# Optimization experiments

Hardware: AMD Instinct MI355X
Metric: run time of the kernel (lower is better)

The kernel has to match this reference:

```python
import jax, jax.numpy as jnp
import numpy as np

B, N, D = 4, 256, 256
H, DH = 4, 64
INNER = H * DH
L, MULT, EDGE, KNN = 2, 2, 11, 3
LN_EPS = 1e-5


def _layernorm(x, w, b):
    m = x.mean(-1, keepdims=True)
    v = ((x - m) ** 2).mean(-1, keepdims=True)
    return (x - m) * jax.lax.rsqrt(v + LN_EPS) * w + b


def _gelu(x):
    return jax.nn.gelu(x, approximate=False)  # torch nn.GELU default = exact erf


def _knn_pair_mask(coords, valid, k):
    # coords [B,M,2], valid [B,M] -> symmetric KNN adjacency among neighbors
    Bm, M = valid.shape
    d = jnp.sqrt(jnp.sum((coords[:, :, None, :] - coords[:, None, :, :]) ** 2, -1))
    eye = jnp.eye(M, dtype=bool)[None]
    inv = ~(valid[:, :, None] & valid[:, None, :])
    d = jnp.where(inv | eye, jnp.inf, d)
    neg, idx = jax.lax.top_k(-d, k)  # k smallest distances
    finite = jnp.isfinite(neg)
    bi = jnp.arange(Bm)[:, None, None]
    ri = jnp.arange(M)[None, :, None]
    mask = jnp.zeros((Bm, M, M), bool).at[bi, ri, idx].set(finite)
    mask = mask | jnp.swapaxes(mask, 1, 2)
    return mask & ~eye


def _build_graph(x, coords):
    # valid node mask (infer_valid_node_mask) and hop ids (infer_hop_ids)
    valid = (jnp.abs(x).sum(-1) > 0).at[:, 0].set(True)
    hop = jnp.ones((B, N), jnp.int32).at[:, 0].set(0)
    hop = hop.at[:, 1 + (N - 1) // 2:].set(2)
    eye = jnp.eye(N, dtype=bool)[None]
    adj = jnp.broadcast_to(eye, (B, N, N))
    nv = valid[:, 1:]
    adj = adj.at[:, 0, 1:].set(nv)
    adj = adj.at[:, 1:, 0].set(nv)
    npm = _knn_pair_mask(coords[:, 1:], nv, min(KNN, N - 2))
    adj = adj.at[:, 1:, 1:].set(adj[:, 1:, 1:] | npm)
    vp = valid[:, :, None] & valid[:, None, :]
    adj = adj & (vp | eye)
    # edge features [B,N,N,11]
    rel = coords[:, None, :, :] - coords[:, :, None, :]  # coords[j]-coords[i]
    dx, dy = rel[..., 0], rel[..., 1]
    dist = jnp.sqrt(dx ** 2 + dy ** 2 + 1e-8)
    cdist = jnp.sqrt(coords[..., 0] ** 2 + coords[..., 1] ** 2 + 1e-8)
    nvm = valid.at[:, 0].set(False)
    cd = jnp.where(nvm, cdist, 0.0)
    cnt = jnp.clip(nvm.sum(-1), 1).astype(x.dtype)
    ls = cd.sum(-1) / cnt
    ls = jnp.where(ls > 0, ls, 1.0)
    ndist = dist / jnp.clip(ls, 1e-6)[:, None, None]
    idx = jnp.arange(N)
    ones2 = jnp.ones((N, N), bool)
    qic = (idx[:, None] == 0) & ones2
    kic = (idx[None, :] == 0) & ones2
    eye2 = jnp.eye(N, dtype=bool)
    isnn = ~(qic | kic | eye2)
    same_hop = hop[:, :, None] == hop[:, None, :]
    hop_delta = jnp.abs(hop[:, None, :] - hop[:, :, None]).astype(x.dtype)
    same_ct = jnp.zeros((B, N, N), x.dtype)  # cell_inf is None
    f = lambda m: jnp.broadcast_to(m.astype(x.dtype), (B, N, N))
    edge_attr = jnp.stack(
        [dx, dy, dist, ndist, f(qic), f(kic), f(eye2), f(isnn),
         same_hop.astype(x.dtype), hop_delta, same_ct], -1)
    return adj, edge_attr


def _forward(x, coords, Wq, Wk, Wv, eb_w1, eb_b1, eb_w2, eb_b2,
             ev_w1, ev_b1, ev_w2, ev_b2, Wo, bo,
             ln1_w, ln1_b, ln2_w, ln2_b, ff_w1, ff_b1, ff_w2, ff_b2):
    adj, e = _build_graph(x, coords)
    scale = DH ** -0.5
    big = jnp.finfo(x.dtype).max
    for l in range(L):
        xn = _layernorm(x, ln1_w[l], ln1_b[l])
        q = (xn @ Wq[l]).reshape(B, N, H, DH).transpose(0, 2, 1, 3)  # b h n d
        k = (xn @ Wk[l]).reshape(B, N, H, DH).transpose(0, 2, 1, 3)
        v = (xn @ Wv[l]).reshape(B, N, H, DH).transpose(0, 2, 1, 3)
        eb = _gelu(e @ eb_w1[l] + eb_b1[l]) @ eb_w2[l] + eb_b2[l]  # [B,N,N,H]
        ev = _gelu(e @ ev_w1[l] + ev_b1[l]) @ ev_w2[l] + ev_b2[l]  # [B,N,N,INNER]
        ev = ev.reshape(B, N, N, H, DH).transpose(0, 3, 1, 2, 4)   # b h i j d
        sim = jnp.einsum('bhid,bhjd->bhij', q, k) * scale + eb.transpose(0, 3, 1, 2)
        sim = jnp.where(adj[:, None], sim, -big)
        attn = jax.nn.softmax(sim, -1)
        msgs = v[:, :, None, :, :] + ev                            # value injection
        out = jnp.einsum('bhij,bhijd->bhid', attn, msgs)
        out = out.transpose(0, 2, 1, 3).reshape(B, N, INNER) @ Wo[l] + bo[l]
        x = x + out
        xn2 = _layernorm(x, ln2_w[l], ln2_b[l])
        hg = xn2 @ ff_w1[l] + ff_b1[l]
        a, g = jnp.split(hg, 2, -1)  # GEGLU
        x = x + ((a * _gelu(g)) @ ff_w2[l] + ff_b2[l])
    return x


def setup_inputs() -> dict:
    key = jax.random.key(0)
    ks = iter(jax.random.split(key, 32))
    w = lambda shape, s=0.05: jax.random.normal(next(ks), shape, jnp.float32) * s
    return {
        'x': jax.random.normal(next(ks), (B, N, D), jnp.float32),
        'coords': jax.random.normal(next(ks), (B, N, 2), jnp.float32) * 3.0,
        'Wq': w((L, D, INNER)), 'Wk': w((L, D, INNER)), 'Wv': w((L, D, INNER)),
        'eb_w1': w((L, EDGE, INNER)), 'eb_b1': jnp.zeros((L, INNER)),
        'eb_w2': w((L, INNER, H)), 'eb_b2': jnp.zeros((L, H)),
        'ev_w1': w((L, EDGE, INNER)), 'ev_b1': jnp.zeros((L, INNER)),
        'ev_w2': w((L, INNER, INNER)), 'ev_b2': jnp.zeros((L, INNER)),
        'Wo': w((L, INNER, D)), 'bo': jnp.zeros((L, D)),
        'ln1_w': jnp.ones((L, D)), 'ln1_b': jnp.zeros((L, D)),
        'ln2_w': jnp.ones((L, D)), 'ln2_b': jnp.zeros((L, D)),
        'ff_w1': w((L, D, 2 * MULT * D)), 'ff_b1': jnp.zeros((L, 2 * MULT * D)),
        'ff_w2': w((L, MULT * D, D)), 'ff_b2': jnp.zeros((L, D)),
    }


def reference(x, coords, Wq, Wk, Wv, eb_w1, eb_b1, eb_w2, eb_b2,
              ev_w1, ev_b1, ev_w2, ev_b2, Wo, bo,
              ln1_w, ln1_b, ln2_w, ln2_b, ff_w1, ff_b1, ff_w2, ff_b2):
    return _forward(x, coords, Wq, Wk, Wv, eb_w1, eb_b1, eb_w2, eb_b2,
                    ev_w1, ev_b1, ev_w2, ev_b2, Wo, bo,
                    ln1_w, ln1_b, ln2_w, ln2_b, ff_w1, ff_b1, ff_w2, ff_b2)
```

## Files before the change

kernel.cpp:

```cpp
#include <hip/hip_runtime.h>


#define MAXE  16384
#define NONX  22080
#define BF16_TOTAL 1441792

typedef __attribute__((ext_vector_type(8))) short bf16x8;
typedef __attribute__((ext_vector_type(4))) float f32x4;

struct PtrPack { const void* p[23]; };

__device__ __forceinline__ float bf2f(unsigned short s) {
  return __uint_as_float(((unsigned)s) << 16);
}
__device__ __forceinline__ unsigned short f2bf(float f) {
  unsigned u = __float_as_uint(f);
  u += 0x7fffu + ((u >> 16) & 1u);
  return (unsigned short)(u >> 16);
}
__device__ __forceinline__ float gelu_f(float x) {
  return 0.5f * x * (1.0f + erff(x * 0.70710678118654752440f));
}
__device__ __forceinline__ float wave_red_sum(float v) {
#pragma unroll
  for (int o = 32; o > 0; o >>= 1) v += __shfl_xor(v, o);
  return v;
}

__device__ __forceinline__ void edge_feats(int i, int j, float cxi, float cyi,
                                           float cxj, float cyj, float lsd, float* e) {
  float dx = cxj - cxi, dy = cyj - cyi;
  float dist = sqrtf(dx * dx + dy * dy + 1e-8f);
  e[0] = dx; e[1] = dy; e[2] = dist; e[3] = dist / lsd;
  bool qic = (i == 0), kic = (j == 0), eye = (i == j);
  e[4] = qic ? 1.f : 0.f;
  e[5] = kic ? 1.f : 0.f;
  e[6] = eye ? 1.f : 0.f;
  e[7] = (!qic && !kic && !eye) ? 1.f : 0.f;
  int hi = (i == 0) ? 0 : ((i < 128) ? 1 : 2);
  int hj = (j == 0) ? 0 : ((j < 128) ? 1 : 2);
  e[8] = (hi == hj) ? 1.f : 0.f;
  int hd = hj - hi;
  e[9] = (float)(hd < 0 ? -hd : hd);
}

__global__ __launch_bounds__(256) void k_convert(PtrPack pp, float* __restrict__ blobF,
                                                 unsigned short* __restrict__ blobB,
                                                 int* __restrict__ valid,
                                                 float* __restrict__ rowsum,
                                                 int* __restrict__ gctr) {
  bool isf32 = (*(const unsigned*)pp.p[15] == 0x3F800000u);
  int t = threadIdx.x;
  if (blockIdx.x == 0 && t == 0) *gctr = 0;
  if (blockIdx.x < 1024) {
    if (blockIdx.x < 32) rowsum[blockIdx.x * 256 + t] = 0.f;
    int r = blockIdx.x;
    int idx = r * 256 + t;
    float v = isf32 ? ((const float*)pp.p[0])[idx]
                    : bf2f(((const unsigned short*)pp.p[0])[idx]);
    blobF[idx] = v;
    __shared__ float s[4];
    float a = wave_red_sum(fabsf(v));
    if ((t & 63) == 0) s[t >> 6] = a;
    __syncthreads();
    if (t == 0) valid[r] = ((s[0] + s[1] + s[2] + s[3]) > 0.0f) || ((r & 255) == 0);
  } else {
    const int fst[16] = {0,2048,7680,8192,10240,10304,15936,16448,16960,17472,17984,18496,19008,19520,21568,22080};
    const int fsz[15] = {2048,5632,512,2048,8,5632,512,512,512,512,512,512,512,2048,512};
    const int fin[15] = {1,5,6,7,8,9,10,12,14,15,16,17,18,20,22};
    const int bst[8]  = {0,131072,262144,393216,524288,655360,1179648,1441792};
    const int bin[7]  = {2,3,4,13,11,19,21};
    const int NUNITS = NONX + BF16_TOTAL / 4;
    for (int u = (blockIdx.x - 1024) * 256 + t; u < NUNITS; u += 1024 * 256) {
      if (u < NONX) {
        int s = 0;
        while (s < 14 && u >= fst[s + 1]) ++s;
        int e = u - fst[s];
        float v = 0.f;
        if (e < fsz[s]) v = isf32 ? ((const float*)pp.p[fin[s]])[e]
                                  : bf2f(((const unsigned short*)pp.p[fin[s]])[e]);
        blobF[262144 + u] = v;
      } else {
        int bi = (u - NONX) * 4;
        int s = 0;
        while (s < 6 && bi >= bst[s + 1]) ++s;
        int e = bi - bst[s];
        ushort4 o;
        if (isf32) {
          const float* sp = (const float*)pp.p[bin[s]] + e;
          o.x = f2bf(sp[0]); o.y = f2bf(sp[1]); o.z = f2bf(sp[2]); o.w = f2bf(sp[3]);
        } else {
          o = *(const ushort4*)((const unsigned short*)pp.p[bin[s]] + e);
        }
        *(ushort4*)&blobB[bi] = o;
      }
    }
  }
}

__global__ __launch_bounds__(256) void k_knn(const float* __restrict__ cf,
                                             const int* __restrict__ valid,
                                             int* __restrict__ knn) {
  int blk = blockIdx.x;
  int b = blk >> 6;
  int w = threadIdx.x >> 6, lane = threadIdx.x & 63;
  int i = (blk & 63) * 4 + w;
  const float2* cc = (const float2*)(cf + b * 512);
  float2 ci = cc[i];
  bool vi = (valid[b * 256 + i] != 0) && (i != 0);
  unsigned long long key[4];
#pragma unroll
  for (int k = 0; k < 4; ++k) {
    int j = lane + 64 * k;
    bool ok = vi && (j != 0) && (j != i) && (valid[b * 256 + j] != 0);
    unsigned long long kk = ~0ull;
    if (ok) {
      float2 cj = cc[j];
      float dx = ci.x - cj.x, dy = ci.y - cj.y;
      float dd = sqrtf(dx * dx + dy * dy);
      kk = (((unsigned long long)__float_as_uint(dd)) << 32) | (unsigned)j;
    }
    key[k] = kk;
  }
  int out[3];
#pragma unroll
  for (int rnd = 0; rnd < 3; ++rnd) {
    unsigned long long m = key[0];
    if (key[1] < m) m = key[1];
    if (key[2] < m) m = key[2];
    if (key[3] < m) m = key[3];
#pragma unroll
    for (int o = 32; o > 0; o >>= 1) {
      unsigned long long om = __shfl_xor(m, o);
      if (om < m) m = om;
    }
    out[rnd] = (m != ~0ull) ? (int)(m & 0xFFFFFFFFull) : -1;
#pragma unroll
    for (int k = 0; k < 4; ++k)
      if (key[k] == m) key[k] = ~0ull;
  }
  if (lane == 0) {
    knn[(b * 256 + i) * 3 + 0] = out[0];
    knn[(b * 256 + i) * 3 + 1] = out[1];
    knn[(b * 256 + i) * 3 + 2] = out[2];
  }
}

__global__ __launch_bounds__(256) void k_csr(const float* __restrict__ cf,
                                             const int* __restrict__ valid,
                                             const int* __restrict__ knn,
                                             float* __restrict__ lsbuf,
                                             int* __restrict__ deg, int* __restrict__ rowptr,
                                             int* __restrict__ rowof, int* __restrict__ colsb,
                                             int* __restrict__ gctr) {
  int b = blockIdx.x, t = threadIdx.x;
  __shared__ unsigned adjw[256][8];
  __shared__ float sred[8];
  __shared__ int wsum[4];
  __shared__ int sbase;

  int r = b * 256 + t;
  float cx = cf[r * 2 + 0], cy = cf[r * 2 + 1];
  int lv = valid[r];
#pragma unroll
  for (int w = 0; w < 8; ++w) adjw[t][w] = 0u;
  __syncthreads();

  atomicOr(&adjw[t][t >> 5], 1u << (t & 31));
  if (t >= 1 && lv) {
    atomicOr(&adjw[0][t >> 5], 1u << (t & 31));
    atomicOr(&adjw[t][0], 1u);
  }
#pragma unroll
  for (int s = 0; s < 3; ++s) {
    int j = knn[r * 3 + s];
    if (j >= 0) {
      atomicOr(&adjw[t][j >> 5], 1u << (j & 31));
      atomicOr(&adjw[j][t >> 5], 1u << (t & 31));
    }
  }
  float cdist = sqrtf(cx * cx + cy * cy + 1e-8f);
  int nvm = (t >= 1) && lv;
  float rs = wave_red_sum(nvm ? cdist : 0.0f);
  float rc = wave_red_sum(nvm ? 1.0f : 0.0f);
  if ((t & 63) == 0) { sred[t >> 6] = rs; sred[4 + (t >> 6)] = rc; }
  __syncthreads();

  if (t == 0) {
    float totd = sred[0] + sred[1] + sred[2] + sred[3];
    float totc = sred[4] + sred[5] + sred[6] + sred[7];
    float ls = totd / fmaxf(totc, 1.0f);
    ls = (ls > 0.0f) ? ls : 1.0f;
    lsbuf[b] = fmaxf(ls, 1e-6f);
  }

  int dg = 0;
#pragma unroll
  for (int w = 0; w < 8; ++w) dg += __popc(adjw[t][w]);

  int lane = t & 63, wv = t >> 6;
  int x = dg;
#pragma unroll
  for (int off = 1; off < 64; off <<= 1) {
    int y = __shfl_up(x, off);
    if (lane >= off) x += y;
  }
  if (lane == 63) wsum[wv] = x;
  __syncthreads();
  if (t == 0) sbase = atomicAdd(gctr, wsum[0] + wsum[1] + wsum[2] + wsum[3]);
  __syncthreads();
  int woff = 0;
#pragma unroll
  for (int k2 = 0; k2 < 4; ++k2) woff += (k2 < wv) ? wsum[k2] : 0;
  int off0 = sbase + woff + x - dg;

  rowptr[r] = off0;
  deg[r] = dg;
  int o = off0;
#pragma unroll
  for (int w = 0; w < 8; ++w) {
    unsigned bits = adjw[t][w];
    while (bits) {
      int bp = __ffs(bits) - 1;
      colsb[o] = w * 32 + bp;
      rowof[o] = r;
      ++o;
      bits &= bits - 1;
    }
  }
}

template <int AMODE, int OMODE>
__device__ __forceinline__ void mfma_body(const void* Aptr, int lda,
                                          const unsigned short* __restrict__ B, int ldb, int n0B,
                                          const float* __restrict__ bias,
                                          const float* resid,
                                          void* C, int ldc, int n0C,
                                          int m0, int K, bool obf,
                                          const float* __restrict__ lnG,
                                          const float* __restrict__ lnB) {
  __shared__ short As[16][72];
  __shared__ short Bs[64][72];
  __shared__ float sG[256], sB2[256];
  int t = threadIdx.x, lane = t & 63, w = t >> 6;

  int am = t >> 3, ak = (t & 7) * 8;
  int bk = t >> 2, bn = (t & 3) * 16;

  f32x4 acc;
  acc[0] = 0.f; acc[1] = 0.f; acc[2] = 0.f; acc[3] = 0.f;

  for (int kc = 0; kc < K; kc += 256) {
    bf16x8 aB[4];
    float4 aF[4][2];
    float4 gF[4][2];
    bf16x8 bR[4][2];
#pragma unroll
    for (int r = 0; r < 4; ++r) {
      int k0 = kc + r * 64;
      if (t < 128) {
        if (AMODE == 0) {
          aB[r] = *(const bf16x8*)((const unsigned short*)Aptr +
                                   (size_t)(m0 + am) * lda + k0 + ak);
        } else {
          const float* ap = (const float*)Aptr + (size_t)(m0 + am) * lda + k0 + ak;
          aF[r][0] = *(const float4*)ap;
          aF[r][1] = *(const float4*)(ap + 4);
          if (AMODE == 1) {
            gF[r][0] = *(const float4*)(ap + 512);
            gF[r][1] = *(const float4*)(ap + 516);
          }
        }
      }
      const unsigned short* bp = B + (size_t)(k0 + bk) * ldb + n0B + bn;
      bR[r][0] = *(const bf16x8*)bp;
      bR[r][1] = *(const bf16x8*)(bp + 8);
    }

    float mm = 0.f, rstd = 0.f;
    if (AMODE == 3) {
      sG[t] = lnG[t]; sB2[t] = lnB[t];
      if (t < 128) {
        float s = 0.f, ss = 0.f;
#pragma unroll
        for (int r = 0; r < 4; ++r)
#pragma unroll
          for (int h2 = 0; h2 < 2; ++h2) {
            float4 v4 = aF[r][h2];
            s += v4.x + v4.y + v4.z + v4.w;
            ss += v4.x * v4.x + v4.y * v4.y + v4.z * v4.z + v4.w * v4.w;
          }
        s += __shfl_xor(s, 1); s += __shfl_xor(s, 2); s += __shfl_xor(s, 4);
        ss += __shfl_xor(ss, 1); ss += __shfl_xor(ss, 2); ss += __shfl_xor(ss, 4);
        mm = s * (1.f / 256.f);
        float var = ss * (1.f / 256.f) - mm * mm;
        rstd = 1.f / sqrtf(var + 1e-5f);
      }
      __syncthreads();
    }

#pragma unroll
    for (int r = 0; r < 4; ++r) {
      if (t < 128) {
        if (AMODE == 0) {
          *(bf16x8*)&As[am][ak] = aB[r];
        } else if (AMODE == 1) {
          float4 a0 = aF[r][0], a1 = aF[r][1];
          float4 g0 = gF[r][0], g1 = gF[r][1];
          short tmp[8];
          tmp[0] = (short)f2bf(a0.x * gelu_f(g0.x));
          tmp[1] = (short)f2bf(a0.y * gelu_f(g0.y));
          tmp[2] = (short)f2bf(a0.z * gelu_f(g0.z));
          tmp[3] = (short)f2bf(a0.w * gelu_f(g0.w));
          tmp[4] = (short)f2bf(a1.x * gelu_f(g1.x));
          tmp[5] = (short)f2bf(a1.y * gelu_f(g1.y));
          tmp[6] = (short)f2bf(a1.z * gelu_f(g1.z));
          tmp[7] = (short)f2bf(a1.w * gelu_f(g1.w));
          *(bf16x8*)&As[am][ak] = *(bf16x8*)tmp;
        } else if (AMODE == 2) {
          float4 a0 = aF[r][0], a1 = aF[r][1];
          short tmp[8];
          tmp[0] = (short)f2bf(a0.x); tmp[1] = (short)f2bf(a0.y);
          tmp[2] = (short)f2bf(a0.z); tmp[3] = (short)f2bf(a0.w);
          tmp[4] = (short)f2bf(a1.x); tmp[5] = (short)f2bf(a1.y);
          tmp[6] = (short)f2bf(a1.z); tmp[7] = (short)f2bf(a1.w);
          *(bf16x8*)&As[am][ak] = *(bf16x8*)tmp;
        } else {
          float4 a0 = aF[r][0], a1 = aF[r][1];
          int kb = kc + r * 64 + ak;
          short tmp[8];
          tmp[0] = (short)f2bf((a0.x - mm) * rstd * sG[kb + 0] + sB2[kb + 0]);
          tmp[1] = (short)f2bf((a0.y - mm) * rstd * sG[kb + 1] + sB2[kb + 1]);
          tmp[2] = (short)f2bf((a0.z - mm) * rstd * sG[kb + 2] + sB2[kb + 2]);
          tmp[3] = (short)f2bf((a0.w - mm) * rstd * sG[kb + 3] + sB2[kb + 3]);
          tmp[4] = (short)f2bf((a1.x - mm) * rstd * sG[kb + 4] + sB2[kb + 4]);
          tmp[5] = (short)f2bf((a1.y - mm) * rstd * sG[kb + 5] + sB2[kb + 5]);
          tmp[6] = (short)f2bf((a1.z - mm) * rstd * sG[kb + 6] + sB2[kb + 6]);
          tmp[7] = (short)f2bf((a1.w - mm) * rstd * sG[kb + 7] + sB2[kb + 7]);
          *(bf16x8*)&As[am][ak] = *(bf16x8*)tmp;
        }
      }
      {
        bf16x8 bv0 = bR[r][0], bv1 = bR[r][1];
#pragma unroll
        for (int i2 = 0; i2 < 8; ++i2) Bs[bn + i2][bk] = bv0[i2];
#pragma unroll
        for (int i2 = 0; i2 < 8; ++i2) Bs[bn + 8 + i2][bk] = bv1[i2];
      }
      __syncthreads();
      int q = lane >> 4;
      bf16x8 af0 = *(const bf16x8*)&As[lane & 15][q * 8];
      bf16x8 af1 = *(const bf16x8*)&As[lane & 15][32 + q * 8];
      bf16x8 bf0 = *(const bf16x8*)&Bs[w * 16 + (lane & 15)][q * 8];
      bf16x8 bf1 = *(const bf16x8*)&Bs[w * 16 + (lane & 15)][32 + q * 8];
      acc = __builtin_amdgcn_mfma_f32_16x16x32_bf16(af0, bf0, acc, 0, 0, 0);
      acc = __builtin_amdgcn_mfma_f32_16x16x32_bf16(af1, bf1, acc, 0, 0, 0);
      __syncthreads();
    }
  }

  int q = lane >> 4;
  int cn = w * 16 + (lane & 15);
  int col = n0C + cn;
  float bv = bias ? bias[n0B + cn] : 0.0f;
#pragma unroll
  for (int rr = 0; rr < 4; ++rr) {
    int row = m0 + q * 4 + rr;
    float v = acc[rr] + bv;
    if (resid) v += resid[(size_t)row * ldc + col];
    if (OMODE == 2 || (OMODE == 1 && obf)) {
      ((unsigned short*)C)[(size_t)row * ldc + col] = f2bf(v);
    } else {
      ((float*)C)[(size_t)row * ldc + col] = v;
    }
  }
}

template <int AMODE, int OMODE>
__global__ __launch_bounds__(256) void k_mfma(const void* A, int lda, int aYoffBytes,
                                              const unsigned short* B, int ldb,
                                              const float* bias, const float* resid,
                                              void* C, int ldc, int K,
                                              const unsigned* probe,
                                              const float* lnG, const float* lnB) {
  bool obf = (OMODE == 1) && probe && (*probe != 0x3F800000u);
  int n0 = blockIdx.y * 64;
  const void* Ap = (const char*)A + (size_t)aYoffBytes * blockIdx.y;
  mfma_body<AMODE, OMODE>(Ap, lda, B, ldb, n0, bias, resid, C, ldc, n0,
                          blockIdx.x * 16, K, obf, lnG, lnB);
}

__global__ __launch_bounds__(256) void k_mfma_qkv(const float* X,
                                                  const float* lnG, const float* lnB,
                                                  const unsigned short* WqL, float* qkv) {
  int sel = blockIdx.y >> 2;
  const unsigned short* B = WqL + sel * 131072;
  int n0B = (blockIdx.y & 3) * 64;
  int n0C = blockIdx.y * 64;
  mfma_body<3, 0>(X, 256, B, 256, n0B, nullptr, nullptr, qkv, 768, n0C,
                  blockIdx.x * 16, 256, false, lnG, lnB);
}

__global__ __launch_bounds__(256) void k_simz(const float* __restrict__ cf,
                                              const float* __restrict__ qkv,
                                              const int* __restrict__ rowof,
                                              const int* __restrict__ colsb,
                                              const int* __restrict__ gctr,
                                              const float* __restrict__ lsbuf,
                                              const float* __restrict__ ebW1,
                                              const float* __restrict__ ebB1,
                                              const float* __restrict__ ebW2,
                                              const float* __restrict__ ebB2,
                                              float* __restrict__ esim,
                                              float* __restrict__ rowsum,
                                              float* __restrict__ tb,
                                              float* __restrict__ vs) {
  int t = threadIdx.x;
  if (blockIdx.x < 4) {
    int hr = blockIdx.x * 256;
    size_t tz = (size_t)hr * 1024 + t;
    tb[tz] = 0.f; tb[tz + 256] = 0.f; tb[tz + 512] = 0.f; tb[tz + 768] = 0.f;
    vs[(size_t)hr * 256 + t] = 0.f;
  }
  int E = *gctr;
  int lane = t & 63, w = t >> 6;
  float W1r[4][10], B1r[4], W2r[4][4];
#pragma unroll
  for (int kk = 0; kk < 4; ++kk) {
    int c = kk * 64 + lane;
    B1r[kk] = ebB1[c];
#pragma unroll
    for (int f = 0; f < 10; ++f) W1r[kk][f] = ebW1[f * 256 + c];
    float4 w2 = *(const float4*)(ebW2 + c * 4);
    W2r[kk][0] = w2.x; W2r[kk][1] = w2.y; W2r[kk][2] = w2.z; W2r[kk][3] = w2.w;
  }
  float b20 = ebB2[0], b21 = ebB2[1], b22 = ebB2[2], b23 = ebB2[3];
  for (int g = blockIdx.x * 4 + w; g < E; g += 4096) {
    int r = rowof[g], j = colsb[g];
    int b = r >> 8, i = r & 255;
    float ls = lsbuf[b];
    const float2* cc = (const float2*)cf;
    float2 ci = cc[b * 256 + i], cj = cc[b * 256 + j];
    float ef[10];
    edge_feats(i, j, ci.x, ci.y, cj.x, cj.y, ls, ef);
    float red[8];
#pragma unroll
    for (int z = 0; z < 8; ++z) red[z] = 0.0f;
#pragma unroll
    for (int kk = 0; kk < 4; ++kk) {
      int c = kk * 64 + lane;
      float h1 = B1r[kk];
#pragma unroll
      for (int f = 0; f < 10; ++f) h1 += ef[f] * W1r[kk][f];
      float g1 = gelu_f(h1);
      red[4] += g1 * W2r[kk][0];
      red[5] += g1 * W2r[kk][1];
      red[6] += g1 * W2r[kk][2];
      red[7] += g1 * W2r[kk][3];
      red[kk] = qkv[(size_t)r * 768 + c] * qkv[((size_t)(b * 256 + j)) * 768 + 256 + c];
    }
#pragma unroll
    for (int z = 0; z < 8; ++z) {
#pragma unroll
      for (int o = 32; o > 0; o >>= 1) red[z] += __shfl_xor(red[z], o);
    }
    if (lane == 0) {
      float e0 = expf(red[0] * 0.125f + red[4] + b20);
      float e1 = expf(red[1] * 0.125f + red[5] + b21);
      float e2 = expf(red[2] * 0.125f + red[6] + b22);
      float e3 = expf(red[3] * 0.125f + red[7] + b23);
      *(float4*)&esim[(size_t)g * 4] = make_float4(e0, e1, e2, e3);
      atomicAdd(&rowsum[r * 4 + 0], e0);
      atomicAdd(&rowsum[r * 4 + 1], e1);
      atomicAdd(&rowsum[r * 4 + 2], e2);
      atomicAdd(&rowsum[r * 4 + 3], e3);
    }
  }
}

__global__ __launch_bounds__(256, 8) void k_accum(const float* __restrict__ cf,
                                                  const float* __restrict__ qkv,
                                                  const int* __restrict__ rowptr,
                                                  const int* __restrict__ deg,
                                                  const int* __restrict__ colsb,
                                                  const float* __restrict__ esim,
                                                  const float* __restrict__ rowsum,
                                                  const float* __restrict__ lsbuf,
                                                  const float* __restrict__ evW1,
                                                  const float* __restrict__ evB1,
                                                  float* __restrict__ tb,
                                                  float* __restrict__ vs) {
  int x = blockIdx.x;
  int r, ch;
  if (x < 1024) { r = x; ch = 0; }
  else { int i5 = x - 1024; r = (i5 / 7) * 256; ch = 1 + i5 % 7; }
  int d = deg[r];
  int e0 = ch * 32;
  if (e0 >= d) return;
  int n = min(32, d - e0);
  bool whole = (ch == 0) && (d <= 32);
  int base = rowptr[r] + e0;
  int b = r >> 8, i = r & 255;
  int u = threadIdx.x, h = u >> 6;

  __shared__ int scols[32];
  __shared__ float4 sattn[32];
  __shared__ float sef[32][10];
  if (u < n) {
    float4 S4 = *(const float4*)&rowsum[r * 4];
    int j = colsb[base + u];
    scols[u] = j;
    float4 e = *(const float4*)&esim[(size_t)(base + u) * 4];
    sattn[u] = make_float4(e.x / S4.x, e.y / S4.y, e.z / S4.z, e.w / S4.w);
    float ls = lsbuf[b];
    const float2* cc = (const float2*)cf;
    float2 ci = cc[b * 256 + i], cj = cc[b * 256 + j];
    float ef[10];
    edge_feats(i, j, ci.x, ci.y, cj.x, cj.y, ls, ef);
#pragma unroll
    for (int f = 0; f < 10; ++f) sef[u][f] = ef[f];
  }
  __syncthreads();

  float evb = evB1[u];
  float w1r[10];
#pragma unroll
  for (int f = 0; f < 10; ++f) w1r[f] = evW1[f * 256 + u];
  float t0 = 0.f, t1 = 0.f, t2 = 0.f, t3 = 0.f, va = 0.f;
#pragma unroll 4
  for (int e = 0; e < n; ++e) {
    float4 a = sattn[e];
    int j = scols[e];
    float h1 = evb;
#pragma unroll
    for (int f = 0; f < 10; ++f) h1 += sef[e][f] * w1r[f];
    float g1 = gelu_f(h1);
    t0 += a.x * g1; t1 += a.y * g1; t2 += a.z * g1; t3 += a.w * g1;
    float ah = (h == 0) ? a.x : (h == 1) ? a.y : (h == 2) ? a.z : a.w;
    va += ah * qkv[((size_t)(b * 256 + j)) * 768 + 512 + u];
  }
  size_t tbase = (size_t)r * 1024 + u;
  if (whole) {
    tb[tbase]       = t0;
    tb[tbase + 256] = t1;
    tb[tbase + 512] = t2;
    tb[tbase + 768] = t3;
    vs[(size_t)r * 256 + u] = va;
  } else {
    atomicAdd(&tb[tbase], t0);
    atomicAdd(&tb[tbase + 256], t1);
    atomicAdd(&tb[tbase + 512], t2);
    atomicAdd(&tb[tbase + 768], t3);
    atomicAdd(&vs[(size_t)r * 256 + u], va);
  }
}

extern "C" void kernel_launch(void* const* d_in, const int* in_sizes, int n_in,
                              void* d_out, int out_size, void* d_ws, size_t ws_size,
                              hipStream_t stream) {
  (void)in_sizes; (void)n_in; (void)out_size; (void)ws_size;

  char* wp = (char*)d_ws;
  auto carve = [&](size_t bytes) -> char* {
    char* p = wp;
    wp += ((bytes + 255) / 256) * 256;
    return p;
  };
  int*   gctr   = (int*)carve(4);
  float* lsb    = (float*)carve(16);
  int*   valid  = (int*)carve(1024 * 4);
  int*   deg    = (int*)carve(1024 * 4);
  int*   rowptr = (int*)carve(1024 * 4);
  int*   rowof  = (int*)carve(MAXE * 4);
  int*   colsb  = (int*)carve(MAXE * 4);
  int*   knn    = (int*)carve(1024 * 3 * 4);
  float* rowsum = (float*)carve(8192 * 4);
  float* sim    = (float*)carve((size_t)MAXE * 16);
  float* blobF  = (float*)carve((size_t)(262144 + NONX) * 4);
  unsigned short* blobB = (unsigned short*)carve((size_t)BF16_TOTAL * 2);
  float* qkv    = (float*)carve((size_t)1024 * 768 * 4);
  float* xcur   = (float*)carve((size_t)262144 * 4);
  float* tb     = (float*)carve((size_t)1048576 * 4);
  float* vs     = (float*)carve((size_t)262144 * 4);
  unsigned short* oi = (unsigned short*)carve((size_t)262144 * 2);

  const float* Xf    = blobF + 0;
  const float* Cf    = blobF + 262144;
  const float* ebW1  = blobF + 264192;
  const float* ebB1  = blobF + 269824;
  const float* ebW2  = blobF + 270336;
  const float* ebB2  = blobF + 272384;
  const float* evW1  = blobF + 272448;
  const float* evB1  = blobF + 278080;
  const float* evB2  = blobF + 278592;
  const float* boB   = blobF + 279104;
  const float* ln1w  = blobF + 279616;
  const float* ln1b  = blobF + 280128;
  const float* ln2w  = blobF + 280640;
  const float* ln2b  = blobF + 281152;
  const float* ffb1  = blobF + 281664;
  const float* ffb2  = blobF + 283712;
  const unsigned short* WqB   = blobB + 0;
  const unsigned short* WoB   = blobB + 393216;
  const unsigned short* evW2B = blobB + 524288;
  const unsigned short* ffw1B = blobB + 655360;
  const unsigned short* ffw2B = blobB + 1179648;

  PtrPack pp;
  for (int i = 0; i < 23; ++i) pp.p[i] = d_in[i];
  const unsigned* probe = (const unsigned*)d_in[15];

  k_convert<<<2048, 256, 0, stream>>>(pp, blobF, blobB, valid, rowsum, gctr);
  k_knn<<<256, 256, 0, stream>>>(Cf, valid, knn);
  k_csr<<<4, 256, 0, stream>>>(Cf, valid, knn, lsb, deg, rowptr, rowof, colsb, gctr);

  for (int l = 0; l < 2; ++l) {
    const float* xsrc = (l == 0) ? Xf : xcur;
    float* rsumL = rowsum + l * 4096;
    k_mfma_qkv<<<dim3(64, 12), 256, 0, stream>>>(xsrc, ln1w + l * 256, ln1b + l * 256,
                                                 WqB + l * 65536, qkv);
    k_simz<<<1024, 256, 0, stream>>>(Cf, qkv, rowof, colsb, gctr, lsb,
                                     ebW1 + l * 2816, ebB1 + l * 256,
                                     ebW2 + l * 1024, ebB2 + l * 4,
                                     sim, rsumL, tb, vs);
    k_accum<<<1052, 256, 0, stream>>>(Cf, qkv, rowptr, deg, colsb, sim, rsumL, lsb,
                                      evW1 + l * 2816, evB1 + l * 256, tb, vs);
    k_mfma<2, 2><<<dim3(64, 4), 256, 0, stream>>>(tb, 1024, 1024, evW2B + l * 65536, 256,
                                                  evB2 + l * 256, vs, oi, 256, 256,
                                                  nullptr, nullptr, nullptr);
    k_mfma<0, 0><<<dim3(64, 4), 256, 0, stream>>>(oi, 256, 0, WoB + l * 65536, 256,
                                                  boB + l * 256, xsrc, xcur, 256, 256,
                                                  nullptr, nullptr, nullptr);
    k_mfma<3, 0><<<dim3(64, 16), 256, 0, stream>>>(xcur, 256, 0, ffw1B + l * 262144, 1024,
                                                   ffb1 + l * 1024, nullptr, tb, 1024, 256,
                                                   nullptr, ln2w + l * 256, ln2b + l * 256);
    if (l == 0) {
      k_mfma<1, 0><<<dim3(64, 4), 256, 0, stream>>>(tb, 1024, 0, ffw2B + l * 131072, 256,
                                                    ffb2 + l * 256, xcur, xcur, 256, 512,
                                                    nullptr, nullptr, nullptr);
    } else {
      k_mfma<1, 1><<<dim3(64, 4), 256, 0, stream>>>(tb, 1024, 0, ffw2B + l * 131072, 256,
                                                    ffb2 + l * 256, xcur, d_out, 256, 512,
                                                    probe, nullptr, nullptr);
    }
  }
}
```

Measured before the change: 289.5 us.

## Fold edge-value W2 into output projection and fuse KNN into CSR build

Precomputes the product of the edge-value second-layer weights with the output projection Wo per head, and concatenates it with Wo, so the two GEMMs (evW2 then Wo) become one GEMM with K=1280 over a combined [tb|vs] buffer. It also moves the KNN search into the CSR kernel as a serial per-thread top-3 scan over shared-memory coordinates, which removes one launch and the knn buffer. The trade-offs are a larger K in the fused GEMM, an extra prep kernel, and a serial 255-iteration loop per thread in a 4-block kernel.

```diff
diff --git a/kernel.cpp b/kernel.cpp
--- a/kernel.cpp
+++ b/kernel.cpp
@@ -98,88 +98,103 @@
   }
 }
 
-__global__ __launch_bounds__(256) void k_knn(const float* __restrict__ cf,
-                                             const int* __restrict__ valid,
-                                             int* __restrict__ knn) {
-  int blk = blockIdx.x;
-  int b = blk >> 6;
-  int w = threadIdx.x >> 6, lane = threadIdx.x & 63;
-  int i = (blk & 63) * 4 + w;
-  const float2* cc = (const float2*)(cf + b * 512);
-  float2 ci = cc[i];
-  bool vi = (valid[b * 256 + i] != 0) && (i != 0);
-  unsigned long long key[4];
-#pragma unroll
-  for (int k = 0; k < 4; ++k) {
-    int j = lane + 64 * k;
-    bool ok = vi && (j != 0) && (j != i) && (valid[b * 256 + j] != 0);
-    unsigned long long kk = ~0ull;
-    if (ok) {
-      float2 cj = cc[j];
-      float dx = ci.x - cj.x, dy = ci.y - cj.y;
-      float dd = sqrtf(dx * dx + dy * dy);
-      kk = (((unsigned long long)__float_as_uint(dd)) << 32) | (unsigned)j;
-    }
-    key[k] = kk;
-  }
-  int out[3];
-#pragma unroll
-  for (int rnd = 0; rnd < 3; ++rnd) {
-    unsigned long long m = key[0];
-    if (key[1] < m) m = key[1];
-    if (key[2] < m) m = key[2];
-    if (key[3] < m) m = key[3];
-#pragma unroll
-    for (int o = 32; o > 0; o >>= 1) {
-      unsigned long long om = __shfl_xor(m, o);
-      if (om < m) m = om;
-    }
-    out[rnd] = (m != ~0ull) ? (int)(m & 0xFFFFFFFFull) : -1;
-#pragma unroll
-    for (int k = 0; k < 4; ++k)
-      if (key[k] == m) key[k] = ~0ull;
-  }
-  if (lane == 0) {
-    knn[(b * 256 + i) * 3 + 0] = out[0];
-    knn[(b * 256 + i) * 3 + 1] = out[1];
-    knn[(b * 256 + i) * 3 + 2] = out[2];
+__global__ __launch_bounds__(256) void k_prep(const unsigned short* __restrict__ evW2B,
+                                              const unsigned short* __restrict__ WoB,
+                                              const float* __restrict__ evB2,
+                                              const float* __restrict__ boB,
+                                              unsigned short* __restrict__ Bcat,
+                                              float* __restrict__ bias2) {
+  int x = blockIdx.x, n = threadIdx.x;
+  if (x < 64) {
+    int l = x >> 5, rem = x & 31;
+    int h = rem >> 3, ug = rem & 7;
+    const unsigned short* W2 = evW2B + l * 65536;
+    const unsigned short* Wo = WoB + l * 65536;
+    __shared__ short sWo[16384];
+    for (int k = n; k < 16384; k += 256) sWo[k] = (short)Wo[h * 64 * 256 + k];
+    __syncthreads();
+    int u0 = ug * 32;
+    for (int u = u0; u < u0 + 32; ++u) {
+      const unsigned short* wrow = W2 + u * 256 + h * 64;
+      float acc = 0.f;
+#pragma unroll 8
+      for (int dh = 0; dh < 64; ++dh)
+        acc += bf2f(wrow[dh]) * bf2f((unsigned short)sWo[dh * 256 + n]);
+      Bcat[(size_t)l * 327680 + (size_t)(h * 256 + u) * 256 + n] = f2bf(acc);
+    }
+  } else if (x < 66) {
+    int l = x - 64;
+    const unsigned short* Wo = WoB + l * 65536;
+    float acc = boB[l * 256 + n];
+    for (int c = 0; c < 256; ++c)
+      acc += evB2[l * 256 + c] * bf2f(Wo[c * 256 + n]);
+    bias2[l * 256 + n] = acc;
+  } else {
+    int idx = x - 66;
+    int l = idx >> 2, q = idx & 3;
+    const unsigned short* Wo = WoB + l * 65536;
+    for (int rr = 0; rr < 64; ++rr) {
+      int c = q * 64 + rr;
+      Bcat[(size_t)l * 327680 + (size_t)(1024 + c) * 256 + n] = Wo[c * 256 + n];
+    }
   }
 }
 
 __global__ __launch_bounds__(256) void k_csr(const float* __restrict__ cf,
                                              const int* __restrict__ valid,
-                                             const int* __restrict__ knn,
                                              float* __restrict__ lsbuf,
                                              int* __restrict__ deg, int* __restrict__ rowptr,
                                              int* __restrict__ rowof, int* __restrict__ colsb,
                                              int* __restrict__ gctr) {
   int b = blockIdx.x, t = threadIdx.x;
   __shared__ unsigned adjw[256][8];
+  __shared__ float2 scc[256];
+  __shared__ int sval[256];
   __shared__ float sred[8];
   __shared__ int wsum[4];
   __shared__ int sbase;
 
   int r = b * 256 + t;
-  float cx = cf[r * 2 + 0], cy = cf[r * 2 + 1];
+  const float2* cc = (const float2*)cf + b * 256;
+  float2 ci = cc[t];
   int lv = valid[r];
+  scc[t] = ci;
+  sval[t] = lv;
 #pragma unroll
   for (int w = 0; w < 8; ++w) adjw[t][w] = 0u;
   __syncthreads();
+
+  unsigned long long k0 = ~0ull, k1 = ~0ull, k2 = ~0ull;
+  if (t != 0 && lv) {
+    for (int j = 1; j < 256; ++j) {
+      if (j == t || !sval[j]) continue;
+      float dx = ci.x - scc[j].x, dy = ci.y - scc[j].y;
+      float dd = sqrtf(dx * dx + dy * dy);
+      unsigned long long kk = (((unsigned long long)__float_as_uint(dd)) << 32) | (unsigned)j;
+      if (kk < k2) {
+        if (kk < k1) {
+          k2 = k1;
+          if (kk < k0) { k1 = k0; k0 = kk; } else k1 = kk;
+        } else k2 = kk;
+      }
+    }
+  }
 
   atomicOr(&adjw[t][t >> 5], 1u << (t & 31));
   if (t >= 1 && lv) {
     atomicOr(&adjw[0][t >> 5], 1u << (t & 31));
     atomicOr(&adjw[t][0], 1u);
   }
+  unsigned long long ks[3] = {k0, k1, k2};
 #pragma unroll
   for (int s = 0; s < 3; ++s) {
-    int j = knn[r * 3 + s];
-    if (j >= 0) {
+    if (ks[s] != ~0ull) {
+      int j = (int)(ks[s] & 0xFFFFFFFFull);
       atomicOr(&adjw[t][j >> 5], 1u << (j & 31));
       atomicOr(&adjw[j][t >> 5], 1u << (t & 31));
     }
   }
-  float cdist = sqrtf(cx * cx + cy * cy + 1e-8f);
+  float cdist = sqrtf(ci.x * ci.x + ci.y * ci.y + 1e-8f);
   int nvm = (t >= 1) && lv;
   float rs = wave_red_sum(nvm ? cdist : 0.0f);
   float rc = wave_red_sum(nvm ? 1.0f : 0.0f);
@@ -211,7 +226,7 @@
   __syncthreads();
   int woff = 0;
 #pragma unroll
-  for (int k2 = 0; k2 < 4; ++k2) woff += (k2 < wv) ? wsum[k2] : 0;
+  for (int k2i = 0; k2i < 4; ++k2i) woff += (k2i < wv) ? wsum[k2i] : 0;
   int off0 = sbase + woff + x - dg;
 
   rowptr[r] = off0;
@@ -413,14 +428,13 @@
                                               const float* __restrict__ ebB2,
                                               float* __restrict__ esim,
                                               float* __restrict__ rowsum,
-                                              float* __restrict__ tb,
-                                              float* __restrict__ vs) {
+                                              float* __restrict__ tbx) {
   int t = threadIdx.x;
   if (blockIdx.x < 4) {
     int hr = blockIdx.x * 256;
-    size_t tz = (size_t)hr * 1024 + t;
-    tb[tz] = 0.f; tb[tz + 256] = 0.f; tb[tz + 512] = 0.f; tb[tz + 768] = 0.f;
-    vs[(size_t)hr * 256 + t] = 0.f;
+    size_t tz = (size_t)hr * 1280 + t;
+    tbx[tz] = 0.f; tbx[tz + 256] = 0.f; tbx[tz + 512] = 0.f;
+    tbx[tz + 768] = 0.f; tbx[tz + 1024] = 0.f;
   }
   int E = *gctr;
   int lane = t & 63, w = t >> 6;
@@ -488,8 +502,7 @@
                                                   const float* __restrict__ lsbuf,
                                                   const float* __restrict__ evW1,
                                                   const float* __restrict__ evB1,
-                                                  float* __restrict__ tb,
-                                                  float* __restrict__ vs) {
+                                                  float* __restrict__ tbx) {
   int x = blockIdx.x;
   int r, ch;
   if (x < 1024) { r = x; ch = 0; }
@@ -539,19 +552,19 @@
     float ah = (h == 0) ? a.x : (h == 1) ? a.y : (h == 2) ? a.z : a.w;
     va += ah * qkv[((size_t)(b * 256 + j)) * 768 + 512 + u];
   }
-  size_t tbase = (size_t)r * 1024 + u;
+  size_t tbase = (size_t)r * 1280 + u;
   if (whole) {
-    tb[tbase]       = t0;
-    tb[tbase + 256] = t1;
-    tb[tbase + 512] = t2;
-    tb[tbase + 768] = t3;
-    vs[(size_t)r * 256 + u] = va;
+    tbx[tbase]        = t0;
+    tbx[tbase + 256]  = t1;
+    tbx[tbase + 512]  = t2;
+    tbx[tbase + 768]  = t3;
+    tbx[tbase + 1024] = va;
   } else {
-    atomicAdd(&tb[tbase], t0);
-    atomicAdd(&tb[tbase + 256], t1);
-    atomicAdd(&tb[tbase + 512], t2);
-    atomicAdd(&tb[tbase + 768], t3);
-    atomicAdd(&vs[(size_t)r * 256 + u], va);
+    atomicAdd(&tbx[tbase], t0);
+    atomicAdd(&tbx[tbase + 256], t1);
+    atomicAdd(&tbx[tbase + 512], t2);
+    atomicAdd(&tbx[tbase + 768], t3);
+    atomicAdd(&tbx[tbase + 1024], va);
   }
 }
 
@@ -573,16 +586,16 @@
   int*   rowptr = (int*)carve(1024 * 4);
   int*   rowof  = (int*)carve(MAXE * 4);
   int*   colsb  = (int*)carve(MAXE * 4);
-  int*   knn    = (int*)carve(1024 * 3 * 4);
   float* rowsum = (float*)carve(8192 * 4);
   float* sim    = (float*)carve((size_t)MAXE * 16);
   float* blobF  = (float*)carve((size_t)(262144 + NONX) * 4);
   unsigned short* blobB = (unsigned short*)carve((size_t)BF16_TOTAL * 2);
+  unsigned short* Bcat  = (unsigned short*)carve((size_t)2 * 327680 * 2);
+  float* bias2  = (float*)carve(512 * 4);
   float* qkv    = (float*)carve((size_t)1024 * 768 * 4);
   float* xcur   = (float*)carve((size_t)262144 * 4);
+  float* tbx    = (float*)carve((size_t)1024 * 1280 * 4);
   float* tb     = (float*)carve((size_t)1048576 * 4);
-  float* vs     = (float*)carve((size_t)262144 * 4);
-  unsigned short* oi = (unsigned short*)carve((size_t)262144 * 2);
 
   const float* Xf    = blobF + 0;
   const float* Cf    = blobF + 262144;
@@ -611,8 +624,8 @@
   const unsigned* probe = (const unsigned*)d_in[15];
 
   k_convert<<<2048, 256, 0, stream>>>(pp, blobF, blobB, valid, rowsum, gctr);
-  k_knn<<<256, 256, 0, stream>>>(Cf, valid, knn);
-  k_csr<<<4, 256, 0, stream>>>(Cf, valid, knn, lsb, deg, rowptr, rowof, colsb, gctr);
+  k_prep<<<74, 256, 0, stream>>>(evW2B, WoB, evB2, boB, Bcat, bias2);
+  k_csr<<<4, 256, 0, stream>>>(Cf, valid, lsb, deg, rowptr, rowof, colsb, gctr);
 
   for (int l = 0; l < 2; ++l) {
     const float* xsrc = (l == 0) ? Xf : xcur;
@@ -622,14 +635,11 @@
     k_simz<<<1024, 256, 0, stream>>>(Cf, qkv, rowof, colsb, gctr, lsb,
                                      ebW1 + l * 2816, ebB1 + l * 256,
                                      ebW2 + l * 1024, ebB2 + l * 4,
-                                     sim, rsumL, tb, vs);
+                                     sim, rsumL, tbx);
     k_accum<<<1052, 256, 0, stream>>>(Cf, qkv, rowptr, deg, colsb, sim, rsumL, lsb,
-                                      evW1 + l * 2816, evB1 + l * 256, tb, vs);
-    k_mfma<2, 2><<<dim3(64, 4), 256, 0, stream>>>(tb, 1024, 1024, evW2B + l * 65536, 256,
-                                                  evB2 + l * 256, vs, oi, 256, 256,
-                                                  nullptr, nullptr, nullptr);
-    k_mfma<0, 0><<<dim3(64, 4), 256, 0, stream>>>(oi, 256, 0, WoB + l * 65536, 256,
-                                                  boB + l * 256, xsrc, xcur, 256, 256,
+                                      evW1 + l * 2816, evB1 + l * 256, tbx);
+    k_mfma<2, 0><<<dim3(64, 4), 256, 0, stream>>>(tbx, 1280, 0, Bcat + l * 327680, 256,
+                                                  bias2 + l * 256, xsrc, xcur, 256, 1280,
                                                   nullptr, nullptr, nullptr);
     k_mfma<3, 0><<<dim3(64, 16), 256, 0, stream>>>(xcur, 256, 0, ffw1B + l * 262144, 1024,
                                                    ffb1 + l * 1024, nullptr, tb, 1024, 256,
```

After: 381.4 us. 1.32x slower.
